# Performance work log

Measured on AMD Instinct MI355X. Metric: run time of the kernel, lower is better.

Reference implementation:

```python
import jax, jax.numpy as jnp
import numpy as np

B, C, Hs, Ws = 2, 256, 64, 64
NQ = Hs * Ws
NH, NP = 8, 8
N_CROSS, N_SELF = 2, 2
FFN = 256
DH = C // NH


def _layernorm(x, g, b, eps=1e-5):
    m = jnp.mean(x, -1, keepdims=True)
    v = jnp.mean((x - m) ** 2, -1, keepdims=True)
    return (x - m) * jax.lax.rsqrt(v + eps) * g + b


def _sine_pos_embed(h, w, num_feats=C // 2, temperature=10000.0):
    # SinePositionEmbedding(d_model//2, normalize=True) on an all-ones mask
    eps = 1e-6
    scale = 2.0 * np.pi
    y = jnp.arange(1, h + 1, dtype=jnp.float32) / (h + eps) * scale
    x = jnp.arange(1, w + 1, dtype=jnp.float32) / (w + eps) * scale
    dim_t = temperature ** (2.0 * (jnp.arange(num_feats) // 2).astype(jnp.float32) / num_feats)
    py = y[:, None] / dim_t  # [h, F]
    px = x[:, None] / dim_t  # [w, F]

    def interleave(p):
        return jnp.stack([jnp.sin(p[:, 0::2]), jnp.cos(p[:, 1::2])], -1).reshape(p.shape[0], -1)

    py = interleave(py)
    px = interleave(px)
    pos = jnp.concatenate([
        jnp.broadcast_to(py[:, None, :], (h, w, num_feats)),
        jnp.broadcast_to(px[None, :, :], (h, w, num_feats)),
    ], -1)
    return pos.reshape(h * w, 2 * num_feats)  # [hw, C]


def _msdeform(query, ref, src, ow, ob, aww, awb, vw, vb, pw, pb):
    # query [B,Lq,C], ref [B,Lq,2] (level dim of 1 squeezed), src [B,Len,C]
    Bq, Lq, _ = query.shape
    Len = src.shape[1]
    value = (src @ vw + vb).reshape(Bq, Len, NH, DH)
    off = (query @ ow + ob).reshape(Bq, Lq, NH, NP, 2)
    aw = jax.nn.softmax((query @ aww + awb).reshape(Bq, Lq, NH, NP), axis=-1)
    norm = jnp.array([Ws, Hs], jnp.float32)
    loc = ref[:, :, None, None, :] + off / norm  # [B,Lq,NH,NP,2], normalized coords
    # grid_sample bilinear, align_corners=False, zero padding
    px = loc[..., 0] * Ws - 0.5
    py = loc[..., 1] * Hs - 0.5
    x0 = jnp.floor(px)
    y0 = jnp.floor(py)
    lx, ly = px - x0, py - y0
    x0i = x0.astype(jnp.int32)
    y0i = y0.astype(jnp.int32)
    v = value.transpose(0, 2, 1, 3)  # [B,NH,Len,DH]

    def corner(xi, yi, w):
        inb = ((xi >= 0) & (xi < Ws) & (yi >= 0) & (yi < Hs)).astype(v.dtype)
        idx = jnp.clip(yi, 0, Hs - 1) * Ws + jnp.clip(xi, 0, Ws - 1)  # [B,Lq,NH,NP]
        idx = idx.transpose(0, 2, 1, 3).reshape(Bq, NH, Lq * NP)
        wT = (w * inb).transpose(0, 2, 1, 3).reshape(Bq, NH, Lq * NP, 1)
        g = jnp.take_along_axis(v, idx[..., None], axis=2)  # [B,NH,Lq*NP,DH]
        return g * wT

    s = (corner(x0i, y0i, (1 - lx) * (1 - ly))
         + corner(x0i + 1, y0i, lx * (1 - ly))
         + corner(x0i, y0i + 1, (1 - lx) * ly)
         + corner(x0i + 1, y0i + 1, lx * ly))  # [B,NH,Lq*NP,DH]
    s = s.reshape(Bq, NH, Lq, NP, DH)
    out = jnp.einsum('bqhp,bhqpd->bqhd', aw, s).reshape(Bq, Lq, C)
    return out @ pw + pb


def _ffn(x, w1, b1, w2, b2):
    return jax.nn.relu(jax.nn.relu(x @ w1 + b1) @ w2 + b2)


def setup_inputs() -> dict:
    key = jax.random.key(0)
    ks = jax.random.split(key, 16)
    s = 0.02
    return {
        'feat0': jax.random.normal(ks[0], (B, C, Hs, Ws), jnp.float32),
        'feat1': jax.random.normal(ks[1], (B, C, Hs, Ws), jnp.float32),
        'query_embed': jax.random.normal(ks[2], (NQ, 2 * C), jnp.float32),
        'ref_w': jax.random.normal(ks[3], (C, 2), jnp.float32) * s,
        'ref_b': jnp.zeros((2,), jnp.float32),
        'fuse_logit': jax.random.normal(ks[4], (2, C), jnp.float32) * s,
        'ln1_g': jnp.ones((4, C), jnp.float32),
        'ln1_b': jnp.zeros((4, C), jnp.float32),
        'off_w': jax.random.normal(ks[5], (4, C, NH * NP * 2), jnp.float32) * s,
        'off_b': jnp.zeros((4, NH * NP * 2), jnp.float32),
        'aw_w': jax.random.normal(ks[6], (4, C, NH * NP), jnp.float32) * s,
        'aw_b': jnp.zeros((4, NH * NP), jnp.float32),
        'val_w': jax.random.normal(ks[7], (4, C, C), jnp.float32) * s,
        'val_b': jnp.zeros((4, C), jnp.float32),
        'out_w': jax.random.normal(ks[8], (4, C, C), jnp.float32) * s,
        'out_b': jnp.zeros((4, C), jnp.float32),
        'ln2_g': jnp.ones((4, C), jnp.float32),
        'ln2_b': jnp.zeros((4, C), jnp.float32),
        'f1_w': jax.random.normal(ks[9], (4, C, FFN), jnp.float32) * s,
        'f1_b': jnp.zeros((4, FFN), jnp.float32),
        'f2_w': jax.random.normal(ks[10], (4, FFN, C), jnp.float32) * s,
        'f2_b': jnp.zeros((4, C), jnp.float32),
    }


def reference(feat0, feat1, query_embed, ref_w, ref_b, fuse_logit, ln1_g, ln1_b,
              off_w, off_b, aw_w, aw_b, val_w, val_b, out_w, out_b,
              ln2_g, ln2_b, f1_w, f1_b, f2_w, f2_b):
    # ModifiedCNW: adaptive per-channel weighted fusion of the two modality maps
    fw = jax.nn.softmax(fuse_logit, axis=0)  # [2, C]
    fused = feat0 * fw[0][None, :, None, None] + feat1 * fw[1][None, :, None, None]
    fused = fused.reshape(B, C, NQ).transpose(0, 2, 1)  # [B, HW, C]

    pos = jnp.broadcast_to(_sine_pos_embed(Hs, Ws)[None], (B, NQ, C))
    qe = jnp.broadcast_to(query_embed[:, :C][None], (B, NQ, C))
    tgt = jnp.broadcast_to(query_embed[:, C:][None], (B, NQ, C))
    ref_pts = jax.nn.sigmoid(qe @ ref_w + ref_b)  # [B, NQ, 2], normalized

    # self-attn reference points are PIXEL coordinates (faithful to source, unnormalized)
    ry, rx = jnp.meshgrid(jnp.linspace(0.5, Hs - 0.5, Hs), jnp.linspace(0.5, Ws - 0.5, Ws), indexing='ij')
    self_ref = jnp.broadcast_to(jnp.stack([rx.reshape(-1), ry.reshape(-1)], -1)[None], (B, NQ, 2))

    for i in range(N_CROSS):
        t2 = _layernorm(tgt, ln1_g[i], ln1_b[i])
        a = _msdeform(t2 + qe, ref_pts, fused, off_w[i], off_b[i], aw_w[i], aw_b[i],
                      val_w[i], val_b[i], out_w[i], out_b[i])
        tgt = tgt + a
        tgt = tgt + _ffn(_layernorm(tgt, ln2_g[i], ln2_b[i]), f1_w[i], f1_b[i], f2_w[i], f2_b[i])

    for j in range(N_SELF):
        i = N_CROSS + j
        # source computes norm1(tgt) but discards it in the self-attn branch
        a = _msdeform(tgt + pos, self_ref, tgt, off_w[i], off_b[i], aw_w[i], aw_b[i],
                      val_w[i], val_b[i], out_w[i], out_b[i])
        tgt = tgt + a
        tgt = tgt + _ffn(_layernorm(tgt, ln2_g[i], ln2_b[i]), f1_w[i], f1_b[i], f2_w[i], f2_b[i])
    return tgt
```

## Files before the change

kernel.cpp:

```cpp
#include <hip/hip_runtime.h>
#include <hip/hip_bf16.h>
#include <math.h>

#define CC   256
#define NQQ  4096
#define MT   8192

typedef __attribute__((ext_vector_type(8))) short s8v;
typedef __attribute__((ext_vector_type(4))) float f4v;

static __device__ __forceinline__ ushort f2bu(float f) {
    __hip_bfloat16 h = __float2bfloat16(f);
    return *reinterpret_cast<ushort*>(&h);
}


__global__ __launch_bounds__(256) void setup_kernel(
        const float* __restrict__ qemb, const float* __restrict__ rw,
        const float* __restrict__ rb,
        const float* __restrict__ feat0, const float* __restrict__ feat1,
        const float* __restrict__ fl,
        const float* __restrict__ val_w, const float* __restrict__ off_w,
        const float* __restrict__ aw_w,  const float* __restrict__ out_w,
        const float* __restrict__ f1_w,  const float* __restrict__ f2_w,
        const float* __restrict__ off_b, const float* __restrict__ aw_b,
        float* __restrict__ pos, float* __restrict__ refp, float* __restrict__ tgt,
        ushort* __restrict__ wval01, ushort* __restrict__ wvalS,
        ushort* __restrict__ woffaw, ushort* __restrict__ wout,
        ushort* __restrict__ wf1, ushort* __restrict__ wf2,
        float* __restrict__ bOA, ushort* __restrict__ fused) {
    __shared__ float tl[64][65];
    int bid = blockIdx.x;
    int t = threadIdx.x;
    if (bid < 2048) {
        int idx = bid * 256 + t;
        int q = idx >> 7, pp = idx & 127;
        int p = pp >> 6, u = pp & 63;
        float coordbase = (p == 0) ? (float)((q >> 6) + 1) : (float)((q & 63) + 1);
        float coord = coordbase * (6.28318530717958647692f / (64.0f + 1e-6f));
        float v = coord * exp2f(-0.20762050593046016f * (float)u);
        *(float2*)(pos + (size_t)q * 256 + p * 128 + u * 2) = make_float2(__sinf(v), __cosf(v));
        return;
    }
    if (bid < 3072) {
        int row = (bid - 2048) * 4 + (t >> 6);
        int l = t & 63;
        float4 v = *(const float4*)(qemb + (size_t)row * 512 + l * 4);
        float a0 = v.x * rw[(l * 4 + 0) * 2] + v.y * rw[(l * 4 + 1) * 2]
                 + v.z * rw[(l * 4 + 2) * 2] + v.w * rw[(l * 4 + 3) * 2];
        float a1 = v.x * rw[(l * 4 + 0) * 2 + 1] + v.y * rw[(l * 4 + 1) * 2 + 1]
                 + v.z * rw[(l * 4 + 2) * 2 + 1] + v.w * rw[(l * 4 + 3) * 2 + 1];
        #pragma unroll
        for (int o = 32; o > 0; o >>= 1) { a0 += __shfl_xor(a0, o); a1 += __shfl_xor(a1, o); }
        if (l == 0) {
            refp[row * 2 + 0] = 1.0f / (1.0f + __expf(-(a0 + rb[0])));
            refp[row * 2 + 1] = 1.0f / (1.0f + __expf(-(a1 + rb[1])));
        }
        return;
    }
    if (bid < 5120) {
        int idx = (bid - 3072) * 256 + t;
        int c4 = idx & 63;
        int q = (idx >> 6) & (NQQ - 1);
        *(float4*)(tgt + (size_t)idx * 4) = *(const float4*)(qemb + (size_t)q * 512 + 256 + c4 * 4);
        return;
    }
    if (bid < 5428) {
        int wb = bid - 5120;
        if (wb >= 304) {
            int layer = wb - 304;
            if (t < 192)
                bOA[layer * 192 + t] = (t < 128) ? off_b[layer * 128 + t]
                                                 : aw_b[layer * 64 + (t - 128)];
            return;
        }
        const float* src; ushort* dstF; int srcStride, ntb, kcb;
        if (wb < 32) {
            int nt = wb & 7, kt = wb >> 3;
            int layer = nt >> 2, nn = (nt & 3) * 64;
            src = val_w + (size_t)layer * 65536 + (size_t)kt * 64 * 256 + nn; srcStride = 256;
            dstF = wval01; ntb = nt * 4; kcb = kt * 2;
        } else if (wb < 64) {
            int b = wb - 32; int layer = b >> 4; int kt = (b >> 2) & 3; int nt = b & 3;
            src = val_w + (size_t)(2 + layer) * 65536 + (size_t)kt * 64 * 256 + nt * 64; srcStride = 256;
            dstF = wvalS + (size_t)layer * 65536; ntb = nt * 4; kcb = kt * 2;
        } else if (wb < 112) {
            int b = wb - 64; int layer = b / 12; int rem = b % 12; int kt = rem / 3; int nt = rem % 3;
            if (nt < 2) { src = off_w + (size_t)layer * 256 * 128 + (size_t)kt * 64 * 128 + nt * 64; srcStride = 128; }
            else        { src = aw_w  + (size_t)layer * 256 * 64  + (size_t)kt * 64 * 64;            srcStride = 64;  }
            dstF = woffaw + (size_t)layer * 49152; ntb = nt * 4; kcb = kt * 2;
        } else {
            int b = wb - 112; int fam = b >> 6; int bb = b & 63;
            int layer = bb >> 4; int kt = (bb >> 2) & 3; int nt = bb & 3;
            const float* s0 = (fam == 0) ? out_w : ((fam == 1) ? f1_w : f2_w);
            ushort* d0      = (fam == 0) ? wout  : ((fam == 1) ? wf1  : wf2);
            src = s0 + (size_t)layer * 65536 + (size_t)kt * 64 * 256 + nt * 64; srcStride = 256;
            dstF = d0 + (size_t)layer * 65536; ntb = nt * 4; kcb = kt * 2;
        }
        int r = t >> 6, c = t & 63;
        #pragma unroll
        for (int rr = 0; rr < 64; rr += 4)
            tl[rr + r][c] = src[(size_t)(rr + r) * srcStride + c];
        __syncthreads();
        int l = t >> 2;
        int e0 = (t & 3) * 2;
        int frow = l & 15;
        int fcol = (l >> 4) * 8;
        #pragma unroll
        for (int s = 0; s < 8; s++) {
            int ntl = s & 3, kcl = s >> 2;
            int ntile = ntb + ntl, kc = kcb + kcl;
            ushort2 val;
            val.x = f2bu(tl[kcl * 32 + fcol + e0    ][ntl * 16 + frow]);
            val.y = f2bu(tl[kcl * 32 + fcol + e0 + 1][ntl * 16 + frow]);
            *(ushort2*)(dstF + (((size_t)ntile * 8 + kc) * 64 + l) * 8 + e0) = val;
        }
        return;
    }
    {
        int fb = bid - 5428;
        int b = fb >> 8;
        int c0 = ((fb >> 6) & 3) * 64;
        int q0 = (fb & 63) * 64;
        int r = t >> 6, c = t & 63;
        #pragma unroll
        for (int rr = 0; rr < 64; rr += 4) {
            int ch = c0 + rr + r;
            float l0 = fl[ch], l1 = fl[CC + ch];
            float m = fmaxf(l0, l1);
            float e0 = __expf(l0 - m), e1 = __expf(l1 - m);
            float inv = 1.0f / (e0 + e1);
            size_t o = ((size_t)b * CC + ch) * NQQ + q0 + c;
            tl[rr + r][c] = (feat0[o] * e0 + feat1[o] * e1) * inv;
        }
        __syncthreads();
        #pragma unroll
        for (int rr = 0; rr < 64; rr += 4)
            fused[((size_t)(b * NQQ + q0 + rr + r)) * CC + c0 + c] = f2bu(tl[c][rr + r]);
    }
}

__global__ __launch_bounds__(1024, 4) void pgemm(const ushort* __restrict__ Abf,
        const ushort* __restrict__ Wf, const float* __restrict__ bias,
        ushort* __restrict__ Cb, int NS) {
    __shared__ ushort Abuf[32 * 264];
    const int t = threadIdx.x;
    const int m0 = blockIdx.x * 32;
    const int cb0 = blockIdx.y * 256;
    const int ntb = blockIdx.y * 16;
    {
        const int rg = t >> 5, c0 = (t & 31) * 8;
        *(int4*)(Abuf + rg * 264 + c0) = *(const int4*)(Abf + (size_t)(m0 + rg) * 256 + c0);
    }
    __syncthreads();
    const int l = t & 63, w = t >> 6;
    const int fr = l & 15, fk8 = (l >> 4) * 8, rb = (l >> 4) * 4;
    f4v acc[2] = {};
    #pragma unroll
    for (int kc = 0; kc < 8; kc++) {
        s8v b = *(const s8v*)(Wf + (((size_t)(ntb + w) * 8 + kc) * 64 + l) * 8);
        s8v a0 = *(const s8v*)(Abuf + fr * 264 + kc * 32 + fk8);
        s8v a1 = *(const s8v*)(Abuf + (16 + fr) * 264 + kc * 32 + fk8);
        acc[0] = __builtin_amdgcn_mfma_f32_16x16x32_bf16(a0, b, acc[0], 0, 0, 0);
        acc[1] = __builtin_amdgcn_mfma_f32_16x16x32_bf16(a1, b, acc[1], 0, 0, 0);
    }
    int gcol = cb0 + w * 16 + fr;
    float bz = bias[gcol];
    #pragma unroll
    for (int g = 0; g < 2; g++)
        #pragma unroll
        for (int r = 0; r < 4; r++)
            Cb[(size_t)(m0 + g * 16 + rb + r) * NS + gcol] = f2bu(acc[g][r] + bz);
}

template<int SELF, int EMITVAL>
__global__ __launch_bounds__(1024, 4) void layer_kernel(
        float* __restrict__ tgt, const float* __restrict__ posq,
        const float* __restrict__ g1, const float* __restrict__ b1,
        const ushort* __restrict__ woffawL, const float* __restrict__ bOAL,
        const ushort* __restrict__ value, int vstride,
        const float* __restrict__ refp,
        const ushort* __restrict__ woutL, const float* __restrict__ out_bL,
        const float* __restrict__ g2, const float* __restrict__ b2,
        const ushort* __restrict__ wf1L, const float* __restrict__ f1_bL,
        const ushort* __restrict__ wf2L, const float* __restrict__ f2_bL,
        const ushort* __restrict__ wvalN, const float* __restrict__ val_bN,
        ushort* __restrict__ valueOut) {
    __shared__ ushort Abuf[32 * 264];
    __shared__ float Slds[32 * 204];
    __shared__ float pred[2][16][32];
    __shared__ float mrs[2][32];
    const int t = threadIdx.x;
    const int m0 = blockIdx.x * 32;

    {
        const int rg = t >> 5, c0 = (t & 31) * 8;
        int m = m0 + rg, q = m & (NQQ - 1);
        const float* src = tgt + (size_t)m * 256 + c0;
        float fv[8];
        *(float4*)&fv[0] = *(const float4*)src;
        *(float4*)&fv[4] = *(const float4*)(src + 4);
        if (!SELF) {
            float s = 0.0f;
            #pragma unroll
            for (int k = 0; k < 8; k++) s += fv[k];
            s += __shfl_xor(s, 1); s += __shfl_xor(s, 2); s += __shfl_xor(s, 4);
            s += __shfl_xor(s, 8); s += __shfl_xor(s, 16);
            float mean = s * (1.0f / 256.0f);
            float s2 = 0.0f;
            #pragma unroll
            for (int k = 0; k < 8; k++) { float d = fv[k] - mean; s2 += d * d; }
            s2 += __shfl_xor(s2, 1); s2 += __shfl_xor(s2, 2); s2 += __shfl_xor(s2, 4);
            s2 += __shfl_xor(s2, 8); s2 += __shfl_xor(s2, 16);
            float rstd = rsqrtf(s2 * (1.0f / 256.0f) + 1e-5f);
            const float* ep = posq + (size_t)q * 512 + c0;
            #pragma unroll
            for (int k = 0; k < 8; k++)
                fv[k] = (fv[k] - mean) * rstd * g1[c0 + k] + b1[c0 + k] + ep[k];
        } else {
            const float* ep = posq + (size_t)q * 256 + c0;
            #pragma unroll
            for (int k = 0; k < 8; k++) fv[k] += ep[k];
        }
        ushort tmp[8];
        #pragma unroll
        for (int k = 0; k < 8; k++) tmp[k] = f2bu(fv[k]);
        *(int4*)(Abuf + rg * 264 + c0) = *(const int4*)tmp;
    }
    __syncthreads();

    const int l = t & 63, w = t >> 6;
    const int fr = l & 15, fk8 = (l >> 4) * 8, rb = (l >> 4) * 4;

    if (w < 12) {
        f4v oacc[2] = {};
        #pragma unroll
        for (int kc = 0; kc < 8; kc++) {
            s8v b = *(const s8v*)(woffawL + (((size_t)w * 8 + kc) * 64 + l) * 8);
            s8v a0 = *(const s8v*)(Abuf + fr * 264 + kc * 32 + fk8);
            s8v a1 = *(const s8v*)(Abuf + (16 + fr) * 264 + kc * 32 + fk8);
            oacc[0] = __builtin_amdgcn_mfma_f32_16x16x32_bf16(a0, b, oacc[0], 0, 0, 0);
            oacc[1] = __builtin_amdgcn_mfma_f32_16x16x32_bf16(a1, b, oacc[1], 0, 0, 0);
        }
        int gcol = w * 16 + fr;
        float bz = bOAL[gcol];
        #pragma unroll
        for (int g = 0; g < 2; g++)
            #pragma unroll
            for (int r = 0; r < 4; r++)
                Slds[(g * 16 + rb + r) * 204 + gcol] = oacc[g][r] + bz;
    }
    __syncthreads();

    {
        const int row = t >> 5, h = (t >> 2) & 7, d8 = t & 3;
        int m = m0 + row, q = m & (NQQ - 1), bidx = m >> 12;
        float rxs, rys;
        if (SELF) { rxs = (float)(q & 63) * 64.0f + 32.0f; rys = (float)(q >> 6) * 64.0f + 32.0f; }
        else      { rxs = refp[q * 2] * 64.0f;             rys = refp[q * 2 + 1] * 64.0f; }
        const float* oa = Slds + row * 204;
        float lg[8];
        #pragma unroll
        for (int p = 0; p < 8; p++) lg[p] = oa[128 + h * 8 + p];
        float mx = lg[0];
        #pragma unroll
        for (int p = 1; p < 8; p++) mx = fmaxf(mx, lg[p]);
        float wg[8], wsum = 0.0f;
        #pragma unroll
        for (int p = 0; p < 8; p++) { wg[p] = __expf(lg[p] - mx); wsum += wg[p]; }
        float inv = 1.0f / wsum;
        const float* offp = oa + h * 16;
        const ushort* vb = value + (size_t)bidx * NQQ * vstride + h * 32 + d8 * 8;
        float acc[8] = {};
        #pragma unroll
        for (int p = 0; p < 8; p++) {
            float px = rxs + offp[p * 2]     - 0.5f;
            float py = rys + offp[p * 2 + 1] - 0.5f;
            float x0f = floorf(px), y0f = floorf(py);
            float lx = px - x0f, ly = py - y0f;
            int x0 = (int)x0f, y0 = (int)y0f;
            float wgt = wg[p] * inv;
            float w00 = (1 - lx) * (1 - ly) * wgt, w10 = lx * (1 - ly) * wgt;
            float w01 = (1 - lx) * ly * wgt,       w11 = lx * ly * wgt;
            #pragma unroll
            for (int cn = 0; cn < 4; cn++) {
                int xi = x0 + (cn & 1), yi = y0 + (cn >> 1);
                float wc = (cn == 0) ? w00 : (cn == 1) ? w10 : (cn == 2) ? w01 : w11;
                if (xi >= 0 && xi < 64 && yi >= 0 && yi < 64) {
                    uint4 uv = *(const uint4*)(vb + (size_t)(yi * 64 + xi) * vstride);
                    uint ua[4] = {uv.x, uv.y, uv.z, uv.w};
                    #pragma unroll
                    for (int k = 0; k < 4; k++) {
                        uint lo = ua[k] << 16;
                        uint hi = ua[k] & 0xffff0000u;
                        acc[k * 2 + 0] += wc * *reinterpret_cast<float*>(&lo);
                        acc[k * 2 + 1] += wc * *reinterpret_cast<float*>(&hi);
                    }
                }
            }
        }
        ushort pk[8];
        #pragma unroll
        for (int k = 0; k < 8; k++) pk[k] = f2bu(acc[k]);
        *(int4*)(Abuf + row * 264 + h * 32 + d8 * 8) = *(const int4*)pk;
    }
    __syncthreads();

    const int gcol = w * 16 + fr;

    float v[2][4];
    {
        f4v acc[2] = {};
        #pragma unroll
        for (int kc = 0; kc < 8; kc++) {
            s8v b = *(const s8v*)(woutL + (((size_t)w * 8 + kc) * 64 + l) * 8);
            s8v a0 = *(const s8v*)(Abuf + fr * 264 + kc * 32 + fk8);
            s8v a1 = *(const s8v*)(Abuf + (16 + fr) * 264 + kc * 32 + fk8);
            acc[0] = __builtin_amdgcn_mfma_f32_16x16x32_bf16(a0, b, acc[0], 0, 0, 0);
            acc[1] = __builtin_amdgcn_mfma_f32_16x16x32_bf16(a1, b, acc[1], 0, 0, 0);
        }
        float ls[2][4], lq[2][4];
        float bz = out_bL[gcol];
        #pragma unroll
        for (int g = 0; g < 2; g++)
            #pragma unroll
            for (int r = 0; r < 4; r++) {
                float tv = tgt[(size_t)(m0 + g * 16 + rb + r) * 256 + gcol] + acc[g][r] + bz;
                v[g][r] = tv;
                ls[g][r] = tv;
                lq[g][r] = tv * tv;
            }
        #pragma unroll
        for (int o = 1; o < 16; o <<= 1)
            #pragma unroll
            for (int g = 0; g < 2; g++)
                #pragma unroll
                for (int r = 0; r < 4; r++) {
                    ls[g][r] += __shfl_xor(ls[g][r], o);
                    lq[g][r] += __shfl_xor(lq[g][r], o);
                }
        if (fr == 0)
            #pragma unroll
            for (int g = 0; g < 2; g++)
                #pragma unroll
                for (int r = 0; r < 4; r++) {
                    pred[0][w][g * 16 + rb + r] = ls[g][r];
                    pred[1][w][g * 16 + rb + r] = lq[g][r];
                }
    }
    __syncthreads();
    if (t < 32) {
        float s = 0.0f, sq = 0.0f;
        #pragma unroll
        for (int ww = 0; ww < 16; ww++) { s += pred[0][ww][t]; sq += pred[1][ww][t]; }
        float mean = s * (1.0f / 256.0f);
        float var = sq * (1.0f / 256.0f) - mean * mean;
        mrs[0][t] = mean;
        mrs[1][t] = rsqrtf(var + 1e-5f);
    }
    __syncthreads();

    #pragma unroll
    for (int g = 0; g < 2; g++)
        #pragma unroll
        for (int r = 0; r < 4; r++) {
            int rloc = g * 16 + rb + r;
            Abuf[rloc * 264 + gcol] = f2bu((v[g][r] - mrs[0][rloc]) * mrs[1][rloc] * g2[gcol] + b2[gcol]);
        }
    __syncthreads();

    {
        f4v acc[2] = {};
        #pragma unroll
        for (int kc = 0; kc < 8; kc++) {
            s8v b = *(const s8v*)(wf1L + (((size_t)w * 8 + kc) * 64 + l) * 8);
            s8v a0 = *(const s8v*)(Abuf + fr * 264 + kc * 32 + fk8);
            s8v a1 = *(const s8v*)(Abuf + (16 + fr) * 264 + kc * 32 + fk8);
            acc[0] = __builtin_amdgcn_mfma_f32_16x16x32_bf16(a0, b, acc[0], 0, 0, 0);
            acc[1] = __builtin_amdgcn_mfma_f32_16x16x32_bf16(a1, b, acc[1], 0, 0, 0);
        }
        __syncthreads();
        float bz = f1_bL[gcol];
        #pragma unroll
        for (int g = 0; g < 2; g++)
            #pragma unroll
            for (int r = 0; r < 4; r++)
                Abuf[(g * 16 + rb + r) * 264 + gcol] = f2bu(fmaxf(acc[g][r] + bz, 0.0f));
    }
    __syncthreads();

    {
        f4v acc[2] = {};
        #pragma unroll
        for (int kc = 0; kc < 8; kc++) {
            s8v b = *(const s8v*)(wf2L + (((size_t)w * 8 + kc) * 64 + l) * 8);
            s8v a0 = *(const s8v*)(Abuf + fr * 264 + kc * 32 + fk8);
            s8v a1 = *(const s8v*)(Abuf + (16 + fr) * 264 + kc * 32 + fk8);
            acc[0] = __builtin_amdgcn_mfma_f32_16x16x32_bf16(a0, b, acc[0], 0, 0, 0);
            acc[1] = __builtin_amdgcn_mfma_f32_16x16x32_bf16(a1, b, acc[1], 0, 0, 0);
        }
        if (EMITVAL) __syncthreads();
        float bz = f2_bL[gcol];
        #pragma unroll
        for (int g = 0; g < 2; g++)
            #pragma unroll
            for (int r = 0; r < 4; r++) {
                float fin = v[g][r] + fmaxf(acc[g][r] + bz, 0.0f);
                tgt[(size_t)(m0 + g * 16 + rb + r) * 256 + gcol] = fin;
                if (EMITVAL) Abuf[(g * 16 + rb + r) * 264 + gcol] = f2bu(fin);
            }
    }
    if (EMITVAL) {
        __syncthreads();
        f4v acc[2] = {};
        #pragma unroll
        for (int kc = 0; kc < 8; kc++) {
            s8v b = *(const s8v*)(wvalN + (((size_t)w * 8 + kc) * 64 + l) * 8);
            s8v a0 = *(const s8v*)(Abuf + fr * 264 + kc * 32 + fk8);
            s8v a1 = *(const s8v*)(Abuf + (16 + fr) * 264 + kc * 32 + fk8);
            acc[0] = __builtin_amdgcn_mfma_f32_16x16x32_bf16(a0, b, acc[0], 0, 0, 0);
            acc[1] = __builtin_amdgcn_mfma_f32_16x16x32_bf16(a1, b, acc[1], 0, 0, 0);
        }
        float bz = val_bN[gcol];
        #pragma unroll
        for (int g = 0; g < 2; g++)
            #pragma unroll
            for (int r = 0; r < 4; r++)
                valueOut[(size_t)(m0 + g * 16 + rb + r) * 256 + gcol] = f2bu(acc[g][r] + bz);
    }
}

extern "C" void kernel_launch(void* const* d_in, const int* in_sizes, int n_in,
                              void* d_out, int out_size, void* d_ws, size_t ws_size,
                              hipStream_t stream) {
    const float* feat0 = (const float*)d_in[0];
    const float* feat1 = (const float*)d_in[1];
    const float* qemb  = (const float*)d_in[2];
    const float* ref_w = (const float*)d_in[3];
    const float* ref_b = (const float*)d_in[4];
    const float* fl    = (const float*)d_in[5];
    const float* ln1_g = (const float*)d_in[6];
    const float* ln1_b = (const float*)d_in[7];
    const float* off_w = (const float*)d_in[8];
    const float* off_b = (const float*)d_in[9];
    const float* aw_w  = (const float*)d_in[10];
    const float* aw_b  = (const float*)d_in[11];
    const float* val_w = (const float*)d_in[12];
    const float* val_b = (const float*)d_in[13];
    const float* out_w = (const float*)d_in[14];
    const float* out_b = (const float*)d_in[15];
    const float* ln2_g = (const float*)d_in[16];
    const float* ln2_b = (const float*)d_in[17];
    const float* f1_w  = (const float*)d_in[18];
    const float* f1_b  = (const float*)d_in[19];
    const float* f2_w  = (const float*)d_in[20];
    const float* f2_b  = (const float*)d_in[21];

    float* tgt = (float*)d_out;
    float* ws = (float*)d_ws;
    float* pos     = ws;
    float* refp    = pos + 1048576;
    float* bOA     = refp + 8192;
    ushort* value01= (ushort*)(bOA + 768);
    ushort* valueS0= value01 + (size_t)MT * 512;
    ushort* valueS1= valueS0 + (size_t)MT * 256;
    ushort* wval01 = valueS1 + (size_t)MT * 256;
    ushort* wvalS  = wval01 + 131072;
    ushort* woffaw = wvalS + 131072;
    ushort* wout   = woffaw + 196608;
    ushort* wf1    = wout + 262144;
    ushort* wf2    = wf1 + 262144;
    ushort* fused_bf = wf2 + 262144;

    setup_kernel<<<5940, 256, 0, stream>>>(qemb, ref_w, ref_b, feat0, feat1, fl,
                                           val_w, off_w, aw_w, out_w, f1_w, f2_w,
                                           off_b, aw_b,
                                           pos, refp, tgt,
                                           wval01, wvalS, woffaw, wout, wf1, wf2,
                                           bOA, fused_bf);

    pgemm<<<dim3(256, 2), 1024, 0, stream>>>(fused_bf, wval01, val_b, value01, 512);

    layer_kernel<0, 0><<<256, 1024, 0, stream>>>(
        tgt, qemb, ln1_g, ln1_b,
        woffaw, bOA, value01, 512, refp,
        wout, out_b, ln2_g, ln2_b,
        wf1, f1_b, wf2, f2_b,
        nullptr, nullptr, nullptr);
    layer_kernel<0, 1><<<256, 1024, 0, stream>>>(
        tgt, qemb, ln1_g + CC, ln1_b + CC,
        woffaw + 49152, bOA + 192, value01 + 256, 512, refp,
        wout + 65536, out_b + CC, ln2_g + CC, ln2_b + CC,
        wf1 + 65536, f1_b + CC, wf2 + 65536, f2_b + CC,
        wvalS, val_b + 2 * CC, valueS0);
    layer_kernel<1, 1><<<256, 1024, 0, stream>>>(
        tgt, pos, nullptr, nullptr,
        woffaw + 2 * 49152, bOA + 2 * 192, valueS0, 256, refp,
        wout + 2 * 65536, out_b + 2 * CC, ln2_g + 2 * CC, ln2_b + 2 * CC,
        wf1 + 2 * 65536, f1_b + 2 * CC, wf2 + 2 * 65536, f2_b + 2 * CC,
        wvalS + 65536, val_b + 3 * CC, valueS1);
    layer_kernel<1, 0><<<256, 1024, 0, stream>>>(
        tgt, pos, nullptr, nullptr,
        woffaw + 3 * 49152, bOA + 3 * 192, valueS1, 256, refp,
        wout + 3 * 65536, out_b + 3 * CC, ln2_g + 3 * CC, ln2_b + 3 * CC,
        wf1 + 3 * 65536, f1_b + 3 * CC, wf2 + 3 * 65536, f2_b + 3 * CC,
        nullptr, nullptr, nullptr);
}
```

Measured before the change: 115.9 us.

## Prefetch next GEMM weights into registers and factor positional embedding tables

The full 4096x256 positional embedding is replaced by two small 64x128 row and column tables, which cuts setup blocks and global traffic. In the layer kernel, each GEMM stage's B-fragment weights are loaded into registers ahead of time, overlapping with the previous stage's compute and barrier. The residual tgt read is also hoisted ahead of a barrier. This raises register pressure under launch_bounds(1024,4), with a risk of spills or reduced occupancy.

```diff
diff --git a/kernel.cpp b/kernel.cpp
--- a/kernel.cpp
+++ b/kernel.cpp
@@ -24,7 +24,8 @@
         const float* __restrict__ aw_w,  const float* __restrict__ out_w,
         const float* __restrict__ f1_w,  const float* __restrict__ f2_w,
         const float* __restrict__ off_b, const float* __restrict__ aw_b,
-        float* __restrict__ pos, float* __restrict__ refp, float* __restrict__ tgt,
+        float* __restrict__ posY, float* __restrict__ posX,
+        float* __restrict__ refp, float* __restrict__ tgt,
         ushort* __restrict__ wval01, ushort* __restrict__ wvalS,
         ushort* __restrict__ woffaw, ushort* __restrict__ wout,
         ushort* __restrict__ wf1, ushort* __restrict__ wf2,
@@ -32,18 +33,21 @@
     __shared__ float tl[64][65];
     int bid = blockIdx.x;
     int t = threadIdx.x;
-    if (bid < 2048) {
+    if (bid < 64) {
         int idx = bid * 256 + t;
-        int q = idx >> 7, pp = idx & 127;
-        int p = pp >> 6, u = pp & 63;
-        float coordbase = (p == 0) ? (float)((q >> 6) + 1) : (float)((q & 63) + 1);
-        float coord = coordbase * (6.28318530717958647692f / (64.0f + 1e-6f));
-        float v = coord * exp2f(-0.20762050593046016f * (float)u);
-        *(float2*)(pos + (size_t)q * 256 + p * 128 + u * 2) = make_float2(__sinf(v), __cosf(v));
+        int tbl = idx >> 13;
+        int rem = idx & 8191;
+        int ci = rem >> 7;
+        int c = rem & 127;
+        int k = c >> 1;
+        float coord = (float)(ci + 1) * (6.28318530717958647692f / (64.0f + 1e-6f));
+        float v = coord * exp2f(-0.20762050593046016f * (float)k);
+        float val = (c & 1) ? __cosf(v) : __sinf(v);
+        (tbl == 0 ? posY : posX)[ci * 128 + c] = val;
         return;
     }
-    if (bid < 3072) {
-        int row = (bid - 2048) * 4 + (t >> 6);
+    if (bid < 1088) {
+        int row = (bid - 64) * 4 + (t >> 6);
         int l = t & 63;
         float4 v = *(const float4*)(qemb + (size_t)row * 512 + l * 4);
         float a0 = v.x * rw[(l * 4 + 0) * 2] + v.y * rw[(l * 4 + 1) * 2]
@@ -58,15 +62,15 @@
         }
         return;
     }
-    if (bid < 5120) {
-        int idx = (bid - 3072) * 256 + t;
+    if (bid < 3136) {
+        int idx = (bid - 1088) * 256 + t;
         int c4 = idx & 63;
         int q = (idx >> 6) & (NQQ - 1);
         *(float4*)(tgt + (size_t)idx * 4) = *(const float4*)(qemb + (size_t)q * 512 + 256 + c4 * 4);
         return;
     }
-    if (bid < 5428) {
-        int wb = bid - 5120;
+    if (bid < 3444) {
+        int wb = bid - 3136;
         if (wb >= 304) {
             int layer = wb - 304;
             if (t < 192)
@@ -118,7 +122,7 @@
         return;
     }
     {
-        int fb = bid - 5428;
+        int fb = bid - 3444;
         int b = fb >> 8;
         int c0 = ((fb >> 6) & 3) * 64;
         int q0 = (fb & 63) * 64;
@@ -176,6 +180,7 @@
 template<int SELF, int EMITVAL>
 __global__ __launch_bounds__(1024, 4) void layer_kernel(
         float* __restrict__ tgt, const float* __restrict__ posq,
+        const float* __restrict__ posY, const float* __restrict__ posX,
         const float* __restrict__ g1, const float* __restrict__ b1,
         const ushort* __restrict__ woffawL, const float* __restrict__ bOAL,
         const ushort* __restrict__ value, int vstride,
@@ -192,6 +197,17 @@
     __shared__ float mrs[2][32];
     const int t = threadIdx.x;
     const int m0 = blockIdx.x * 32;
+    const int l = t & 63, w = t >> 6;
+    const int fr = l & 15, fk8 = (l >> 4) * 8, rb = (l >> 4) * 4;
+    const int gcol = w * 16 + fr;
+
+    s8v breg[8];
+    {
+        int nt = (w < 12) ? w : 0;
+        #pragma unroll
+        for (int kc = 0; kc < 8; kc++)
+            breg[kc] = *(const s8v*)(woffawL + (((size_t)nt * 8 + kc) * 64 + l) * 8);
+    }
 
     {
         const int rg = t >> 5, c0 = (t & 31) * 8;
@@ -218,7 +234,8 @@
             for (int k = 0; k < 8; k++)
                 fv[k] = (fv[k] - mean) * rstd * g1[c0 + k] + b1[c0 + k] + ep[k];
         } else {
-            const float* ep = posq + (size_t)q * 256 + c0;
+            const float* ep = (c0 < 128) ? (posY + (q >> 6) * 128 + c0)
+                                         : (posX + (q & 63) * 128 + (c0 - 128));
             #pragma unroll
             for (int k = 0; k < 8; k++) fv[k] += ep[k];
         }
@@ -229,29 +246,32 @@
     }
     __syncthreads();
 
-    const int l = t & 63, w = t >> 6;
-    const int fr = l & 15, fk8 = (l >> 4) * 8, rb = (l >> 4) * 4;
-
-    if (w < 12) {
+    {
         f4v oacc[2] = {};
-        #pragma unroll
-        for (int kc = 0; kc < 8; kc++) {
-            s8v b = *(const s8v*)(woffawL + (((size_t)w * 8 + kc) * 64 + l) * 8);
-            s8v a0 = *(const s8v*)(Abuf + fr * 264 + kc * 32 + fk8);
-            s8v a1 = *(const s8v*)(Abuf + (16 + fr) * 264 + kc * 32 + fk8);
-            oacc[0] = __builtin_amdgcn_mfma_f32_16x16x32_bf16(a0, b, oacc[0], 0, 0, 0);
-            oacc[1] = __builtin_amdgcn_mfma_f32_16x16x32_bf16(a1, b, oacc[1], 0, 0, 0);
-        }
-        int gcol = w * 16 + fr;
-        float bz = bOAL[gcol];
-        #pragma unroll
-        for (int g = 0; g < 2; g++)
-            #pragma unroll
-            for (int r = 0; r < 4; r++)
-                Slds[(g * 16 + rb + r) * 204 + gcol] = oacc[g][r] + bz;
-    }
-    __syncthreads();
-
+        if (w < 12) {
+            #pragma unroll
+            for (int kc = 0; kc < 8; kc++) {
+                s8v a0 = *(const s8v*)(Abuf + fr * 264 + kc * 32 + fk8);
+                s8v a1 = *(const s8v*)(Abuf + (16 + fr) * 264 + kc * 32 + fk8);
+                oacc[0] = __builtin_amdgcn_mfma_f32_16x16x32_bf16(a0, breg[kc], oacc[0], 0, 0, 0);
+                oacc[1] = __builtin_amdgcn_mfma_f32_16x16x32_bf16(a1, breg[kc], oacc[1], 0, 0, 0);
+            }
+        }
+        #pragma unroll
+        for (int kc = 0; kc < 8; kc++)
+            breg[kc] = *(const s8v*)(woutL + (((size_t)w * 8 + kc) * 64 + l) * 8);
+        if (w < 12) {
+            float bz = bOAL[gcol];
+            #pragma unroll
+            for (int g = 0; g < 2; g++)
+                #pragma unroll
+                for (int r = 0; r < 4; r++)
+                    Slds[(g * 16 + rb + r) * 204 + gcol] = oacc[g][r] + bz;
+        }
+    }
+    __syncthreads();
+
+    float tres[2][4];
     {
         const int row = t >> 5, h = (t >> 2) & 7, d8 = t & 3;
         int m = m0 + row, q = m & (NQQ - 1), bidx = m >> 12;
@@ -303,29 +323,34 @@
         #pragma unroll
         for (int k = 0; k < 8; k++) pk[k] = f2bu(acc[k]);
         *(int4*)(Abuf + row * 264 + h * 32 + d8 * 8) = *(const int4*)pk;
-    }
-    __syncthreads();
-
-    const int gcol = w * 16 + fr;
+        #pragma unroll
+        for (int g = 0; g < 2; g++)
+            #pragma unroll
+            for (int r = 0; r < 4; r++)
+                tres[g][r] = tgt[(size_t)(m0 + g * 16 + rb + r) * 256 + gcol];
+    }
+    __syncthreads();
 
     float v[2][4];
     {
         f4v acc[2] = {};
         #pragma unroll
         for (int kc = 0; kc < 8; kc++) {
-            s8v b = *(const s8v*)(woutL + (((size_t)w * 8 + kc) * 64 + l) * 8);
             s8v a0 = *(const s8v*)(Abuf + fr * 264 + kc * 32 + fk8);
             s8v a1 = *(const s8v*)(Abuf + (16 + fr) * 264 + kc * 32 + fk8);
-            acc[0] = __builtin_amdgcn_mfma_f32_16x16x32_bf16(a0, b, acc[0], 0, 0, 0);
-            acc[1] = __builtin_amdgcn_mfma_f32_16x16x32_bf16(a1, b, acc[1], 0, 0, 0);
-        }
+            acc[0] = __builtin_amdgcn_mfma_f32_16x16x32_bf16(a0, breg[kc], acc[0], 0, 0, 0);
+            acc[1] = __builtin_amdgcn_mfma_f32_16x16x32_bf16(a1, breg[kc], acc[1], 0, 0, 0);
+        }
+        #pragma unroll
+        for (int kc = 0; kc < 8; kc++)
+            breg[kc] = *(const s8v*)(wf1L + (((size_t)w * 8 + kc) * 64 + l) * 8);
         float ls[2][4], lq[2][4];
         float bz = out_bL[gcol];
         #pragma unroll
         for (int g = 0; g < 2; g++)
             #pragma unroll
             for (int r = 0; r < 4; r++) {
-                float tv = tgt[(size_t)(m0 + g * 16 + rb + r) * 256 + gcol] + acc[g][r] + bz;
+                float tv = tres[g][r] + acc[g][r] + bz;
                 v[g][r] = tv;
                 ls[g][r] = tv;
                 lq[g][r] = tv * tv;
@@ -373,12 +398,14 @@
         f4v acc[2] = {};
         #pragma unroll
         for (int kc = 0; kc < 8; kc++) {
-            s8v b = *(const s8v*)(wf1L + (((size_t)w * 8 + kc) * 64 + l) * 8);
             s8v a0 = *(const s8v*)(Abuf + fr * 264 + kc * 32 + fk8);
             s8v a1 = *(const s8v*)(Abuf + (16 + fr) * 264 + kc * 32 + fk8);
-            acc[0] = __builtin_amdgcn_mfma_f32_16x16x32_bf16(a0, b, acc[0], 0, 0, 0);
-            acc[1] = __builtin_amdgcn_mfma_f32_16x16x32_bf16(a1, b, acc[1], 0, 0, 0);
-        }
+            acc[0] = __builtin_amdgcn_mfma_f32_16x16x32_bf16(a0, breg[kc], acc[0], 0, 0, 0);
+            acc[1] = __builtin_amdgcn_mfma_f32_16x16x32_bf16(a1, breg[kc], acc[1], 0, 0, 0);
+        }
+        #pragma unroll
+        for (int kc = 0; kc < 8; kc++)
+            breg[kc] = *(const s8v*)(wf2L + (((size_t)w * 8 + kc) * 64 + l) * 8);
         __syncthreads();
         float bz = f1_bL[gcol];
         #pragma unroll
@@ -393,13 +420,17 @@
         f4v acc[2] = {};
         #pragma unroll
         for (int kc = 0; kc < 8; kc++) {
-            s8v b = *(const s8v*)(wf2L + (((size_t)w * 8 + kc) * 64 + l) * 8);
             s8v a0 = *(const s8v*)(Abuf + fr * 264 + kc * 32 + fk8);
             s8v a1 = *(const s8v*)(Abuf + (16 + fr) * 264 + kc * 32 + fk8);
-            acc[0] = __builtin_amdgcn_mfma_f32_16x16x32_bf16(a0, b, acc[0], 0, 0, 0);
-            acc[1] = __builtin_amdgcn_mfma_f32_16x16x32_bf16(a1, b, acc[1], 0, 0, 0);
-        }
-        if (EMITVAL) __syncthreads();
+            acc[0] = __builtin_amdgcn_mfma_f32_16x16x32_bf16(a0, breg[kc], acc[0], 0, 0, 0);
+            acc[1] = __builtin_amdgcn_mfma_f32_16x16x32_bf16(a1, breg[kc], acc[1], 0, 0, 0);
+        }
+        if (EMITVAL) {
+            #pragma unroll
+            for (int kc = 0; kc < 8; kc++)
+                breg[kc] = *(const s8v*)(wvalN + (((size_t)w * 8 + kc) * 64 + l) * 8);
+            __syncthreads();
+        }
         float bz = f2_bL[gcol];
         #pragma unroll
         for (int g = 0; g < 2; g++)
@@ -415,11 +446,10 @@
         f4v acc[2] = {};
         #pragma unroll
         for (int kc = 0; kc < 8; kc++) {
-            s8v b = *(const s8v*)(wvalN + (((size_t)w * 8 + kc) * 64 + l) * 8);
             s8v a0 = *(const s8v*)(Abuf + fr * 264 + kc * 32 + fk8);
             s8v a1 = *(const s8v*)(Abuf + (16 + fr) * 264 + kc * 32 + fk8);
-            acc[0] = __builtin_amdgcn_mfma_f32_16x16x32_bf16(a0, b, acc[0], 0, 0, 0);
-            acc[1] = __builtin_amdgcn_mfma_f32_16x16x32_bf16(a1, b, acc[1], 0, 0, 0);
+            acc[0] = __builtin_amdgcn_mfma_f32_16x16x32_bf16(a0, breg[kc], acc[0], 0, 0, 0);
+            acc[1] = __builtin_amdgcn_mfma_f32_16x16x32_bf16(a1, breg[kc], acc[1], 0, 0, 0);
         }
         float bz = val_bN[gcol];
         #pragma unroll
@@ -458,8 +488,9 @@
 
     float* tgt = (float*)d_out;
     float* ws = (float*)d_ws;
-    float* pos     = ws;
-    float* refp    = pos + 1048576;
+    float* posY    = ws;
+    float* posX    = posY + 8192;
+    float* refp    = posX + 8192;
     float* bOA     = refp + 8192;
     ushort* value01= (ushort*)(bOA + 768);
     ushort* valueS0= value01 + (size_t)MT * 512;
@@ -472,35 +503,35 @@
     ushort* wf2    = wf1 + 262144;
     ushort* fused_bf = wf2 + 262144;
 
-    setup_kernel<<<5940, 256, 0, stream>>>(qemb, ref_w, ref_b, feat0, feat1, fl,
+    setup_kernel<<<3956, 256, 0, stream>>>(qemb, ref_w, ref_b, feat0, feat1, fl,
                                            val_w, off_w, aw_w, out_w, f1_w, f2_w,
                                            off_b, aw_b,
-                                           pos, refp, tgt,
+                                           posY, posX, refp, tgt,
                                            wval01, wvalS, woffaw, wout, wf1, wf2,
                                            bOA, fused_bf);
 
     pgemm<<<dim3(256, 2), 1024, 0, stream>>>(fused_bf, wval01, val_b, value01, 512);
 
     layer_kernel<0, 0><<<256, 1024, 0, stream>>>(
-        tgt, qemb, ln1_g, ln1_b,
+        tgt, qemb, posY, posX, ln1_g, ln1_b,
         woffaw, bOA, value01, 512, refp,
         wout, out_b, ln2_g, ln2_b,
         wf1, f1_b, wf2, f2_b,
         nullptr, nullptr, nullptr);
     layer_kernel<0, 1><<<256, 1024, 0, stream>>>(
-        tgt, qemb, ln1_g + CC, ln1_b + CC,
+        tgt, qemb, posY, posX, ln1_g + CC, ln1_b + CC,
         woffaw + 49152, bOA + 192, value01 + 256, 512, refp,
         wout + 65536, out_b + CC, ln2_g + CC, ln2_b + CC,
         wf1 + 65536, f1_b + CC, wf2 + 65536, f2_b + CC,
         wvalS, val_b + 2 * CC, valueS0);
     layer_kernel<1, 1><<<256, 1024, 0, stream>>>(
-        tgt, pos, nullptr, nullptr,
+        tgt, nullptr, posY, posX, nullptr, nullptr,
         woffaw + 2 * 49152, bOA + 2 * 192, valueS0, 256, refp,
         wout + 2 * 65536, out_b + 2 * CC, ln2_g + 2 * CC, ln2_b + 2 * CC,
         wf1 + 2 * 65536, f1_b + 2 * CC, wf2 + 2 * 65536, f2_b + 2 * CC,
         wvalS + 65536, val_b + 3 * CC, valueS1);
     layer_kernel<1, 0><<<256, 1024, 0, stream>>>(
-        tgt, pos, nullptr, nullptr,
+        tgt, nullptr, posY, posX, nullptr, nullptr,
         woffaw + 3 * 49152, bOA + 3 * 192, valueS1, 256, refp,
         wout + 3 * 65536, out_b + 3 * CC, ln2_g + 3 * CC, ln2_b + 3 * CC,
         wf1 + 3 * 65536, f1_b + 3 * CC, wf2 + 3 * 65536, f2_b + 3 * CC,
```

After: 121.8 us. 5.1% more time.
